# Performance work log

Measured on AMD Instinct MI355X. Metric: run time of the kernel, lower is better.

## Reference

```python
import jax, jax.numpy as jnp
import numpy as np

NUM_SAMPLES = 4_194_304  # 2**22 samples (~87s @ 48kHz) -> memory-bound streaming IIR


def setup_inputs() -> dict:
    key = jax.random.key(0)
    k1, k2 = jax.random.split(key)
    # [attack, decay, filter_lp, filter_hp, gain]; uniform(0,1) is in the valid clamped range
    parameters = jax.random.uniform(k1, (5,), dtype=jnp.float32)
    noise = jax.random.normal(k2, (NUM_SAMPLES,), dtype=jnp.float32)
    return {"parameters": parameters, "noise": noise}


def _one_pole_lowpass(x, c):
    # y[n] = (1 - c) * x[n] + c * y[n-1]
    def step(y_prev, xn):
        y = (1.0 - c) * xn + c * y_prev
        return y, y
    _, y = jax.lax.scan(step, jnp.zeros((), x.dtype), x)
    return y


def _one_pole_highpass(x, c):
    # y[n] = c * (y[n-1] + x[n] - x[n-1])
    dx = jnp.concatenate([x[:1], x[1:] - x[:-1]])
    def step(y_prev, d):
        y = c * (y_prev + d)
        return y, y
    _, y = jax.lax.scan(step, jnp.zeros((), x.dtype), dx)
    return y


def reference(parameters, noise):
    attack = jnp.clip(parameters[0], 1e-7, None)
    decay = jnp.clip(parameters[1], 1e-7, None)
    filter_lp = jnp.clip(parameters[2], 1e-7, 0.99)
    filter_hp = jnp.clip(parameters[3], 1e-7, 0.99)
    gain = jnp.clip(parameters[4], 1e-7, None)

    n = noise.shape[0]
    t = jnp.linspace(0.0, 1.0, n, dtype=noise.dtype)  # matches registered 'time' buffer
    # exponential attack/decay envelope
    envelope = (1.0 - jnp.exp(-t / attack)) * jnp.exp(-t / decay)

    filtered = _one_pole_lowpass(noise, filter_lp)
    filtered = _one_pole_highpass(filtered, filter_hp)
    return filtered * envelope * gain
```

## Files before the change

kernel.cpp:

```cpp
#include <hip/hip_runtime.h>
#include <math.h>


#define BLOCK 256
#define CHUNK 21
#define TWORDS (BLOCK * CHUNK)
#define HALO   1280
#define SAMP   (TWORDS - HALO)

typedef float vfloat4 __attribute__((ext_vector_type(4)));

struct Op { float a, w, b; };
__device__ __forceinline__ Op opmul(Op A, Op B) {
    Op C;
    C.a = A.a * B.a;
    C.w = fmaf(A.w, B.a, A.b * B.w);
    C.b = A.b * B.b;
    return C;
}

__global__ __launch_bounds__(BLOCK) void noisegen_kernel(
    const float* __restrict__ params,
    const float* __restrict__ noise,
    float* __restrict__ out, int n)
{
    __shared__ __align__(16) float xs[TWORDS];
    __shared__ float swy[4], swz[4];

    float attack = fmaxf(params[0], 1e-7f);
    float decay  = fmaxf(params[1], 1e-7f);
    float a      = fminf(fmaxf(params[2], 1e-7f), 0.99f);
    float b      = fminf(fmaxf(params[3], 1e-7f), 0.99f);
    float gain   = fmaxf(params[4], 1e-7f);
    float omc    = 1.0f - a;

    int tid  = threadIdx.x;
    int B    = blockIdx.x * SAMP;
    int base = B - HALO;

    for (int v = tid; v < (TWORDS >> 2); v += BLOCK) {
        int i = v << 2;
        int g = base + i;
        vfloat4 val;
        if (g >= 0 && g + 4 <= n) {
            val = *(const vfloat4*)(noise + g);
        } else {
            val.x = (g     >= 0 && g     < n) ? noise[g]     : 0.0f;
            val.y = (g + 1 >= 0 && g + 1 < n) ? noise[g + 1] : 0.0f;
            val.z = (g + 2 >= 0 && g + 2 < n) ? noise[g + 2] : 0.0f;
            val.w = (g + 3 >= 0 && g + 3 < n) ? noise[g + 3] : 0.0f;
        }
        *(vfloat4*)(xs + i) = val;
    }
    __syncthreads();

    int l0 = tid * CHUNK;
    float yv = 0.0f, zv = 0.0f;
    #pragma unroll 3
    for (int j = 0; j < CHUNK; ++j) {
        float x  = xs[l0 + j];
        float yn = fmaf(a, yv, omc * x);
        zv = b * (zv + (yn - yv));
        yv = yn;
        xs[l0 + j] = zv;
    }

    int lane = tid & 63, wid = tid >> 6;
    Op m1 = { a, b * (a - 1.0f), b };
    Op m2 = opmul(m1, m1), m4 = opmul(m2, m2), m8 = opmul(m4, m4), m16 = opmul(m8, m8);
    Op P = opmul(opmul(m16, m4), m1);

    Op Psave[6];
    float cy = yv, cz = zv;
    #pragma unroll
    for (int k = 0; k < 6; ++k) {
        Psave[k] = P;
        int d = 1 << k;
        float py = __shfl_up(cy, d, 64);
        float pz = __shfl_up(cz, d, 64);
        if (lane >= d) {
            cy = fmaf(P.a, py, cy);
            cz = fmaf(P.w, py, fmaf(P.b, pz, cz));
        }
        P = opmul(P, P);
    }
    if (lane == 63) { swy[wid] = cy; swz[wid] = cz; }
    __syncthreads();

    float pry = 0.0f, prz = 0.0f;
    for (int u = 0; u < wid; ++u) {
        float ny = fmaf(P.a, pry, swy[u]);
        float nz = fmaf(P.w, pry, fmaf(P.b, prz, swz[u]));
        pry = ny; prz = nz;
    }
    float ey = __shfl_up(cy, 1, 64);
    float ez = __shfl_up(cz, 1, 64);
    if (lane == 0) { ey = 0.0f; ez = 0.0f; }
    Op O = { 1.0f, 0.0f, 1.0f };
    #pragma unroll
    for (int k = 0; k < 6; ++k)
        if ((lane >> k) & 1) O = opmul(Psave[k], O);
    float y0 = fmaf(O.a, pry, ey);
    float z0 = ez + fmaf(O.w, pry, O.b * prz);

    float inv_nm1 = 1.0f / (float)(n - 1);
    float ia = -1.0f / attack;
    float id = -1.0f / decay;
    float t0 = (float)(base + l0) * inv_nm1;
    float ea = __expf(ia * t0);
    float ed = __expf(id * t0);
    float ra = __expf(ia * inv_nm1);
    float rd = __expf(id * inv_nm1);

    float yh = y0, zh = z0;
    #pragma unroll 3
    for (int j = 0; j < CHUNK; ++j) {
        float yn = a * yh;
        zh = b * (zh + (yn - yh));
        yh = yn;
        int li = l0 + j;
        if (base + li == 0) { ea = 1.0f; ed = 1.0f; }
        if (li >= HALO) {
            float env = (1.0f - ea) * ed;
            xs[li] = (xs[li] + zh) * (env * gain);
        }
        ea *= ra; ed *= rd;
    }
    __syncthreads();

    for (int v = tid; v < (SAMP >> 2); v += BLOCK) {
        int i = v << 2;
        int g = B + i;
        if (g + 4 <= n) {
            vfloat4 val = *(const vfloat4*)(xs + HALO + i);
            __builtin_nontemporal_store(val, (vfloat4*)(out + g));
        } else {
            for (int c = 0; c < 4; ++c)
                if (g + c < n) out[g + c] = xs[HALO + i + c];
        }
    }
}

extern "C" void kernel_launch(void* const* d_in, const int* in_sizes, int n_in,
                              void* d_out, int out_size, void* d_ws, size_t ws_size,
                              hipStream_t stream) {
    const float* params = (const float*)d_in[0];
    const float* noise  = (const float*)d_in[1];
    float* out = (float*)d_out;
    int n = in_sizes[1];
    int grid = (n + SAMP - 1) / SAMP;
    noisegen_kernel<<<grid, BLOCK, 0, stream>>>(params, noise, out, n);
}
```

Before: 75.45 us.

## Replace halo-based approximate scan with exact two-pass block-carry IIR scan

Drops the 1280-sample halo recomputation and shared-memory staging. A first kernel computes per-block end states and stores them to a workspace. A second kernel combines all preceding block carries exactly, using powers of the transition operator spread across threads, then recomputes the filter and writes output from registers. This removes the redundant halo reads and LDS traffic, but reads the input twice, adds a second launch, and adds an O(blocks) carry gather per block.

```diff
diff --git a/kernel.cpp b/kernel.cpp
--- a/kernel.cpp
+++ b/kernel.cpp
@@ -3,12 +3,14 @@
 
 
 #define BLOCK 256
-#define CHUNK 21
-#define TWORDS (BLOCK * CHUNK)
-#define HALO   1280
-#define SAMP   (TWORDS - HALO)
+#define CHUNK 16
+#define SAMP  (BLOCK * CHUNK)
+#define ESTG_CAP 4096
 
 typedef float vfloat4 __attribute__((ext_vector_type(4)));
+typedef float vfloat2 __attribute__((ext_vector_type(2)));
+
+__device__ float Est_g[ESTG_CAP];
 
 struct Op { float a, w, b; };
 __device__ __forceinline__ Op opmul(Op A, Op B) {
@@ -19,62 +21,75 @@
     return C;
 }
 
-__global__ __launch_bounds__(BLOCK) void noisegen_kernel(
+template<bool EMIT>
+__global__ __launch_bounds__(BLOCK, 4) void ng_kernel(
     const float* __restrict__ params,
     const float* __restrict__ noise,
-    float* __restrict__ out, int n)
+    float* __restrict__ out,
+    float* __restrict__ EstArg,
+    int n)
 {
-    __shared__ __align__(16) float xs[TWORDS];
-    __shared__ float swy[4], swz[4];
-
-    float attack = fmaxf(params[0], 1e-7f);
-    float decay  = fmaxf(params[1], 1e-7f);
-    float a      = fminf(fmaxf(params[2], 1e-7f), 0.99f);
-    float b      = fminf(fmaxf(params[3], 1e-7f), 0.99f);
-    float gain   = fmaxf(params[4], 1e-7f);
-    float omc    = 1.0f - a;
-
-    int tid  = threadIdx.x;
-    int B    = blockIdx.x * SAMP;
-    int base = B - HALO;
-
-    for (int v = tid; v < (TWORDS >> 2); v += BLOCK) {
-        int i = v << 2;
-        int g = base + i;
-        vfloat4 val;
-        if (g >= 0 && g + 4 <= n) {
-            val = *(const vfloat4*)(noise + g);
-        } else {
-            val.x = (g     >= 0 && g     < n) ? noise[g]     : 0.0f;
-            val.y = (g + 1 >= 0 && g + 1 < n) ? noise[g + 1] : 0.0f;
-            val.z = (g + 2 >= 0 && g + 2 < n) ? noise[g + 2] : 0.0f;
-            val.w = (g + 3 >= 0 && g + 3 < n) ? noise[g + 3] : 0.0f;
-        }
-        *(vfloat4*)(xs + i) = val;
-    }
-    __syncthreads();
-
-    int l0 = tid * CHUNK;
+    __shared__ float swy[4], swz[4], ry[4], rz[4];
+
+    float* __restrict__ Est = EstArg ? EstArg : Est_g;
+
+    const int tid  = threadIdx.x;
+    const int lane = tid & 63;
+    const int wid  = tid >> 6;
+    const int b    = blockIdx.x;
+    const int g0   = b * SAMP + tid * CHUNK;
+
+    const float a   = fminf(fmaxf(params[2], 1e-7f), 0.99f);
+    const float bb  = fminf(fmaxf(params[3], 1e-7f), 0.99f);
+    const float omc = 1.0f - a;
+
+    int nt = 0;
+    vfloat2 Ev[4] = {{0.f,0.f},{0.f,0.f},{0.f,0.f},{0.f,0.f}};
+    if (EMIT) {
+        int em = b - 1 - tid;
+        nt = (em >= 0) ? ((em >> 8) + 1) : 0;
+        #pragma unroll
+        for (int j = 0; j < 4; ++j) {
+            if (j < nt) {
+                int u = b - 1 - tid - (j << 8);
+                Ev[j] = *(const vfloat2*)(Est + 2 * u);
+            }
+        }
+    }
+
+    vfloat4 xq[4];
+    if (g0 + CHUNK <= n) {
+        #pragma unroll
+        for (int q = 0; q < 4; ++q)
+            xq[q] = *(const vfloat4*)(noise + g0 + 4 * q);
+    } else {
+        #pragma unroll
+        for (int q = 0; q < 4; ++q) {
+            #pragma unroll
+            for (int c = 0; c < 4; ++c) {
+                int g = g0 + 4 * q + c;
+                xq[q][c] = (g < n) ? noise[g] : 0.0f;
+            }
+        }
+    }
+
     float yv = 0.0f, zv = 0.0f;
-    #pragma unroll 3
+    #pragma unroll
     for (int j = 0; j < CHUNK; ++j) {
-        float x  = xs[l0 + j];
+        float x  = xq[j >> 2][j & 3];
         float yn = fmaf(a, yv, omc * x);
-        zv = b * (zv + (yn - yv));
+        zv = bb * (zv + (yn - yv));
         yv = yn;
-        xs[l0 + j] = zv;
-    }
-
-    int lane = tid & 63, wid = tid >> 6;
-    Op m1 = { a, b * (a - 1.0f), b };
-    Op m2 = opmul(m1, m1), m4 = opmul(m2, m2), m8 = opmul(m4, m4), m16 = opmul(m8, m8);
-    Op P = opmul(opmul(m16, m4), m1);
-
-    Op Psave[6];
+    }
+
+    Op m1 = { a, bb * (a - 1.0f), bb };
+    Op m2 = opmul(m1, m1), m4 = opmul(m2, m2), m8 = opmul(m4, m4);
+    Op P  = opmul(m8, m8);
+    Op O  = { 1.0f, 0.0f, 1.0f };
     float cy = yv, cz = zv;
     #pragma unroll
     for (int k = 0; k < 6; ++k) {
-        Psave[k] = P;
+        if (EMIT && ((lane >> k) & 1)) O = opmul(P, O);
         int d = 1 << k;
         float py = __shfl_up(cy, d, 64);
         float pz = __shfl_up(cz, d, 64);
@@ -93,50 +108,103 @@
         float nz = fmaf(P.w, pry, fmaf(P.b, prz, swz[u]));
         pry = ny; prz = nz;
     }
+
+    if (!EMIT) {
+        if (tid == 255) {
+            vfloat2 e;
+            e.x = fmaf(P.a, pry, cy);
+            e.y = fmaf(P.w, pry, fmaf(P.b, prz, cz));
+            *(vfloat2*)(Est + 2 * b) = e;
+        }
+        return;
+    }
+
     float ey = __shfl_up(cy, 1, 64);
     float ez = __shfl_up(cz, 1, 64);
     if (lane == 0) { ey = 0.0f; ez = 0.0f; }
-    Op O = { 1.0f, 0.0f, 1.0f };
-    #pragma unroll
-    for (int k = 0; k < 6; ++k)
-        if ((lane >> k) & 1) O = opmul(Psave[k], O);
-    float y0 = fmaf(O.a, pry, ey);
-    float z0 = ez + fmaf(O.w, pry, O.b * prz);
-
-    float inv_nm1 = 1.0f / (float)(n - 1);
-    float ia = -1.0f / attack;
-    float id = -1.0f / decay;
-    float t0 = (float)(base + l0) * inv_nm1;
+
+    Op R2 = opmul(P, P);
+    Op Q  = opmul(R2, R2);
+    Op Ot = { 1.0f, 0.0f, 1.0f };
+    Op cur = Q;
+    #pragma unroll
+    for (int k = 0; k < 8; ++k) {
+        if ((tid >> k) & 1) Ot = opmul(cur, Ot);
+        cur = opmul(cur, cur);
+    }
+    float Hy = 0.0f, Hz = 0.0f;
+    for (int j = nt - 1; j >= 4; --j) {
+        int u = b - 1 - tid - (j << 8);
+        vfloat2 e = *(const vfloat2*)(Est + 2 * u);
+        float t = fmaf(cur.a, Hy, e.x);
+        Hz = fmaf(cur.w, Hy, fmaf(cur.b, Hz, e.y));
+        Hy = t;
+    }
+    #pragma unroll
+    for (int j = 3; j >= 0; --j) {
+        if (j < nt) {
+            float t = fmaf(cur.a, Hy, Ev[j].x);
+            Hz = fmaf(cur.w, Hy, fmaf(cur.b, Hz, Ev[j].y));
+            Hy = t;
+        }
+    }
+    float vy = Ot.a * Hy;
+    float vz = fmaf(Ot.w, Hy, Ot.b * Hz);
+    #pragma unroll
+    for (int d = 1; d < 64; d <<= 1) {
+        vy += __shfl_xor(vy, d, 64);
+        vz += __shfl_xor(vz, d, 64);
+    }
+    if (lane == 0) { ry[wid] = vy; rz[wid] = vz; }
+    __syncthreads();
+    float s0y = (ry[0] + ry[1]) + (ry[2] + ry[3]);
+    float s0z = (rz[0] + rz[1]) + (rz[2] + rz[3]);
+
+    float wy = s0y, wz = s0z;
+    for (int u = 0; u < wid; ++u) {
+        float t = P.a * wy;
+        wz = fmaf(P.w, wy, P.b * wz);
+        wy = t;
+    }
+    wy += pry; wz += prz;
+    float y0 = fmaf(O.a, wy, ey);
+    float z0 = ez + fmaf(O.w, wy, O.b * wz);
+
+    const float attack = fmaxf(params[0], 1e-7f);
+    const float decay  = fmaxf(params[1], 1e-7f);
+    const float gain   = fmaxf(params[4], 1e-7f);
+    const float inv    = 1.0f / (float)(n - 1);
+    const float ia = -1.0f / attack;
+    const float id = -1.0f / decay;
+    const float t0 = (float)g0 * inv;
     float ea = __expf(ia * t0);
-    float ed = __expf(id * t0);
-    float ra = __expf(ia * inv_nm1);
-    float rd = __expf(id * inv_nm1);
-
-    float yh = y0, zh = z0;
-    #pragma unroll 3
+    float ed = __expf(id * t0) * gain;
+    const float ra = __expf(ia * inv);
+    const float rd = __expf(id * inv);
+
+    vfloat4 oq[4];
+    yv = y0; zv = z0;
+    #pragma unroll
     for (int j = 0; j < CHUNK; ++j) {
-        float yn = a * yh;
-        zh = b * (zh + (yn - yh));
-        yh = yn;
-        int li = l0 + j;
-        if (base + li == 0) { ea = 1.0f; ed = 1.0f; }
-        if (li >= HALO) {
-            float env = (1.0f - ea) * ed;
-            xs[li] = (xs[li] + zh) * (env * gain);
-        }
+        float x  = xq[j >> 2][j & 3];
+        float yn = fmaf(a, yv, omc * x);
+        zv = bb * (zv + (yn - yv));
+        yv = yn;
+        oq[j >> 2][j & 3] = zv * ((1.0f - ea) * ed);
         ea *= ra; ed *= rd;
     }
-    __syncthreads();
-
-    for (int v = tid; v < (SAMP >> 2); v += BLOCK) {
-        int i = v << 2;
-        int g = B + i;
-        if (g + 4 <= n) {
-            vfloat4 val = *(const vfloat4*)(xs + HALO + i);
-            __builtin_nontemporal_store(val, (vfloat4*)(out + g));
-        } else {
-            for (int c = 0; c < 4; ++c)
-                if (g + c < n) out[g + c] = xs[HALO + i + c];
+    if (g0 + CHUNK <= n) {
+        #pragma unroll
+        for (int q = 0; q < 4; ++q)
+            *(vfloat4*)(out + g0 + 4 * q) = oq[q];
+    } else {
+        #pragma unroll
+        for (int q = 0; q < 4; ++q) {
+            #pragma unroll
+            for (int c = 0; c < 4; ++c) {
+                int g = g0 + 4 * q + c;
+                if (g < n) out[g] = oq[q][c];
+            }
         }
     }
 }
@@ -149,5 +217,8 @@
     float* out = (float*)d_out;
     int n = in_sizes[1];
     int grid = (n + SAMP - 1) / SAMP;
-    noisegen_kernel<<<grid, BLOCK, 0, stream>>>(params, noise, out, n);
+    float* Est = (ws_size >= (size_t)(2 * grid) * sizeof(float))
+                     ? (float*)d_ws : nullptr;
+    ng_kernel<false><<<grid, BLOCK, 0, stream>>>(params, noise, out, Est, n);
+    ng_kernel<true ><<<grid, BLOCK, 0, stream>>>(params, noise, out, Est, n);
 }
```

Result: slower. 80.54 us (+6.7%).

## Keep per-thread chunk in registers instead of LDS staging

Applied to the files above, without the earlier changes.

Removes the shared-memory tile: each thread loads its 20-sample chunk directly from global memory as five float4 vectors, runs the filter in registers, and writes output straight to global with nontemporal stores. CHUNK changes from 21 to 20 so chunks align to 16 bytes. Halo threads exit early after the scan, and the prefix-operator composition is folded into the scan loop. Per-thread strided float4 accesses are less coalesced than the old block-cooperative copies, and fewer output samples per block means more redundant halo work.

```diff
diff --git a/kernel.cpp b/kernel.cpp
--- a/kernel.cpp
+++ b/kernel.cpp
@@ -3,9 +3,9 @@
 
 
 #define BLOCK 256
-#define CHUNK 21
+#define CHUNK 20
+#define HALO  1280
 #define TWORDS (BLOCK * CHUNK)
-#define HALO   1280
 #define SAMP   (TWORDS - HALO)
 
 typedef float vfloat4 __attribute__((ext_vector_type(4)));
@@ -19,62 +19,57 @@
     return C;
 }
 
-__global__ __launch_bounds__(BLOCK) void noisegen_kernel(
+__global__ __launch_bounds__(BLOCK) void ng_halo(
     const float* __restrict__ params,
     const float* __restrict__ noise,
     float* __restrict__ out, int n)
 {
-    __shared__ __align__(16) float xs[TWORDS];
     __shared__ float swy[4], swz[4];
 
-    float attack = fmaxf(params[0], 1e-7f);
-    float decay  = fmaxf(params[1], 1e-7f);
-    float a      = fminf(fmaxf(params[2], 1e-7f), 0.99f);
-    float b      = fminf(fmaxf(params[3], 1e-7f), 0.99f);
-    float gain   = fmaxf(params[4], 1e-7f);
-    float omc    = 1.0f - a;
+    const int tid  = threadIdx.x;
+    const int lane = tid & 63;
+    const int wid  = tid >> 6;
+    const int base = blockIdx.x * SAMP - HALO;
+    const int g0   = base + tid * CHUNK;
 
-    int tid  = threadIdx.x;
-    int B    = blockIdx.x * SAMP;
-    int base = B - HALO;
+    const float a   = fminf(fmaxf(params[2], 1e-7f), 0.99f);
+    const float bb  = fminf(fmaxf(params[3], 1e-7f), 0.99f);
+    const float omc = 1.0f - a;
 
-    for (int v = tid; v < (TWORDS >> 2); v += BLOCK) {
-        int i = v << 2;
-        int g = base + i;
-        vfloat4 val;
-        if (g >= 0 && g + 4 <= n) {
-            val = *(const vfloat4*)(noise + g);
-        } else {
-            val.x = (g     >= 0 && g     < n) ? noise[g]     : 0.0f;
-            val.y = (g + 1 >= 0 && g + 1 < n) ? noise[g + 1] : 0.0f;
-            val.z = (g + 2 >= 0 && g + 2 < n) ? noise[g + 2] : 0.0f;
-            val.w = (g + 3 >= 0 && g + 3 < n) ? noise[g + 3] : 0.0f;
+    vfloat4 xq[5];
+    if (g0 >= 0 && g0 + CHUNK <= n) {
+        #pragma unroll
+        for (int q = 0; q < 5; ++q)
+            xq[q] = *(const vfloat4*)(noise + g0 + 4 * q);
+    } else {
+        #pragma unroll
+        for (int q = 0; q < 5; ++q) {
+            #pragma unroll
+            for (int c = 0; c < 4; ++c) {
+                int g = g0 + 4 * q + c;
+                xq[q][c] = (g >= 0 && g < n) ? noise[g] : 0.0f;
+            }
         }
-        *(vfloat4*)(xs + i) = val;
-    }
-    __syncthreads();
-
-    int l0 = tid * CHUNK;
-    float yv = 0.0f, zv = 0.0f;
-    #pragma unroll 3
-    for (int j = 0; j < CHUNK; ++j) {
-        float x  = xs[l0 + j];
-        float yn = fmaf(a, yv, omc * x);
-        zv = b * (zv + (yn - yv));
-        yv = yn;
-        xs[l0 + j] = zv;
     }
 
-    int lane = tid & 63, wid = tid >> 6;
-    Op m1 = { a, b * (a - 1.0f), b };
+    float yv = 0.0f, zv = 0.0f;
+    #pragma unroll
+    for (int j = 0; j < CHUNK; ++j) {
+        float x  = xq[j >> 2][j & 3];
+        float yn = fmaf(a, yv, omc * x);
+        zv = bb * (zv + (yn - yv));
+        yv = yn;
+        xq[j >> 2][j & 3] = zv;
+    }
+
+    Op m1 = { a, bb * (a - 1.0f), bb };
     Op m2 = opmul(m1, m1), m4 = opmul(m2, m2), m8 = opmul(m4, m4), m16 = opmul(m8, m8);
-    Op P = opmul(opmul(m16, m4), m1);
-
-    Op Psave[6];
+    Op P  = opmul(m16, m4);
+    Op O  = { 1.0f, 0.0f, 1.0f };
     float cy = yv, cz = zv;
     #pragma unroll
     for (int k = 0; k < 6; ++k) {
-        Psave[k] = P;
+        if ((lane >> k) & 1) O = opmul(P, O);
         int d = 1 << k;
         float py = __shfl_up(cy, d, 64);
         float pz = __shfl_up(cz, d, 64);
@@ -85,7 +80,14 @@
         P = opmul(P, P);
     }
     if (lane == 63) { swy[wid] = cy; swz[wid] = cz; }
+
+    float ey = __shfl_up(cy, 1, 64);
+    float ez = __shfl_up(cz, 1, 64);
+    if (lane == 0) { ey = 0.0f; ez = 0.0f; }
+
     __syncthreads();
+
+    if (tid < HALO / CHUNK) return;
 
     float pry = 0.0f, prz = 0.0f;
     for (int u = 0; u < wid; ++u) {
@@ -93,50 +95,44 @@
         float nz = fmaf(P.w, pry, fmaf(P.b, prz, swz[u]));
         pry = ny; prz = nz;
     }
-    float ey = __shfl_up(cy, 1, 64);
-    float ez = __shfl_up(cz, 1, 64);
-    if (lane == 0) { ey = 0.0f; ez = 0.0f; }
-    Op O = { 1.0f, 0.0f, 1.0f };
+
+    float yh = fmaf(O.a, pry, ey);
+    float zh = ez + fmaf(O.w, pry, O.b * prz);
+
+    const float attack = fmaxf(params[0], 1e-7f);
+    const float decay  = fmaxf(params[1], 1e-7f);
+    const float gain   = fmaxf(params[4], 1e-7f);
+    const float inv    = 1.0f / (float)(n - 1);
+    const float ia = -1.0f / attack;
+    const float id = -1.0f / decay;
+    const float t0 = (float)g0 * inv;
+    float ea = __expf(ia * t0);
+    float ed = __expf(id * t0) * gain;
+    const float ra = __expf(ia * inv);
+    const float rd = __expf(id * inv);
+
     #pragma unroll
-    for (int k = 0; k < 6; ++k)
-        if ((lane >> k) & 1) O = opmul(Psave[k], O);
-    float y0 = fmaf(O.a, pry, ey);
-    float z0 = ez + fmaf(O.w, pry, O.b * prz);
-
-    float inv_nm1 = 1.0f / (float)(n - 1);
-    float ia = -1.0f / attack;
-    float id = -1.0f / decay;
-    float t0 = (float)(base + l0) * inv_nm1;
-    float ea = __expf(ia * t0);
-    float ed = __expf(id * t0);
-    float ra = __expf(ia * inv_nm1);
-    float rd = __expf(id * inv_nm1);
-
-    float yh = y0, zh = z0;
-    #pragma unroll 3
     for (int j = 0; j < CHUNK; ++j) {
         float yn = a * yh;
-        zh = b * (zh + (yn - yh));
+        zh = bb * (zh + (yn - yh));
         yh = yn;
-        int li = l0 + j;
-        if (base + li == 0) { ea = 1.0f; ed = 1.0f; }
-        if (li >= HALO) {
-            float env = (1.0f - ea) * ed;
-            xs[li] = (xs[li] + zh) * (env * gain);
-        }
+        float zt = xq[j >> 2][j & 3] + zh;
+        xq[j >> 2][j & 3] = zt * ((1.0f - ea) * ed);
         ea *= ra; ed *= rd;
     }
-    __syncthreads();
 
-    for (int v = tid; v < (SAMP >> 2); v += BLOCK) {
-        int i = v << 2;
-        int g = B + i;
-        if (g + 4 <= n) {
-            vfloat4 val = *(const vfloat4*)(xs + HALO + i);
-            __builtin_nontemporal_store(val, (vfloat4*)(out + g));
-        } else {
-            for (int c = 0; c < 4; ++c)
-                if (g + c < n) out[g + c] = xs[HALO + i + c];
+    if (g0 + CHUNK <= n) {
+        #pragma unroll
+        for (int q = 0; q < 5; ++q)
+            __builtin_nontemporal_store(xq[q], (vfloat4*)(out + g0 + 4 * q));
+    } else {
+        #pragma unroll
+        for (int q = 0; q < 5; ++q) {
+            #pragma unroll
+            for (int c = 0; c < 4; ++c) {
+                int g = g0 + 4 * q + c;
+                if (g < n) out[g] = xq[q][c];
+            }
         }
     }
 }
@@ -149,5 +145,5 @@
     float* out = (float*)d_out;
     int n = in_sizes[1];
     int grid = (n + SAMP - 1) / SAMP;
-    noisegen_kernel<<<grid, BLOCK, 0, stream>>>(params, noise, out, n);
+    ng_halo<<<grid, BLOCK, 0, stream>>>(params, noise, out, n);
 }
```

Measured after the change: 84.82 us. +12.4%, slower.
